# Kernel tuning notes

Hardware: AMD Instinct MI355X
Metric: run time of the kernel (lower is better)

## Reference

```python
import jax, jax.numpy as jnp
import numpy as np
import math

B, N, DIM = 4, 4096, 1024
HEADS, DHEAD, NRF = 16, 64, 64
STAB = 1e-6  # numerical_stabilizer


def setup_inputs() -> dict:
    key = jax.random.key(0)
    k1, k2, k3, k4 = jax.random.split(key, 4)
    x = jax.random.normal(k1, (B, N, DIM), dtype=jnp.float32)
    W_qkv = jax.random.normal(k2, (DIM, 3 * HEADS * DHEAD), dtype=jnp.float32) * (1.0 / math.sqrt(DIM))
    RF = jax.random.normal(k3, (HEADS, DHEAD, NRF), dtype=jnp.float32) / math.sqrt(NRF)
    W_out = jax.random.normal(k4, (HEADS * DHEAD, DIM), dtype=jnp.float32) * (1.0 / math.sqrt(HEADS * DHEAD))
    b_out = jnp.zeros((DIM,), dtype=jnp.float32)
    return {"x": x, "W_qkv": W_qkv, "RF": RF, "W_out": W_out, "b_out": b_out}


def _phi(t, RF):
    # kernel transformation: project onto random features, then ReLU (default kernel)
    return jax.nn.relu(jnp.einsum('bhnd,hdr->bhnr', t, RF))


def reference(x, W_qkv, RF, W_out, b_out):
    b, n, _ = x.shape
    qkv = x @ W_qkv                                  # [b, n, 3*h*d]
    q, k, v = jnp.split(qkv, 3, axis=-1)
    def to_heads(t):
        return t.reshape(b, n, HEADS, DHEAD).transpose(0, 2, 1, 3)  # [b,h,n,d]
    q, k, v = to_heads(q), to_heads(k), to_heads(v)

    phi_q = _phi(q, RF)                              # [b,h,n,r]
    phi_k = _phi(k, RF)                              # [b,h,n,r]

    # linear-complexity FAVOR+ attention
    kv = jnp.einsum('bhnr,bhnd->bhrd', phi_k, v)     # [b,h,r,d]
    out = jnp.einsum('bhnr,bhrd->bhnd', phi_q, kv)   # [b,h,n,d]
    # normalizer: einsum('bhnr,bhmr->bhn') == phi_q @ sum_m(phi_k)
    k_sum = phi_k.sum(axis=2)                        # [b,h,r]
    normalizer = jnp.einsum('bhnr,bhr->bhn', phi_q, k_sum)[..., None] + STAB
    out = out / normalizer

    out = out.transpose(0, 2, 1, 3).reshape(b, n, HEADS * DHEAD)
    out = out @ W_out + b_out
    return out
```

## Files before the change

### kernel.cpp

```cpp
#include <hip/hip_runtime.h>


typedef __attribute__((ext_vector_type(8))) short s8v;
typedef __attribute__((ext_vector_type(4))) short s4v;
typedef __attribute__((ext_vector_type(4))) float f4v;
typedef __attribute__((ext_vector_type(4))) int   i4v;

#define MFMA16(a, b, c) __builtin_amdgcn_mfma_f32_16x16x32_bf16((a), (b), (c), 0, 0, 0)

__device__ __forceinline__ unsigned short f2bf(float f) {
  unsigned int u = __builtin_bit_cast(unsigned int, f);
  unsigned int r = (u + 0x7FFFu + ((u >> 16) & 1u)) >> 16;
  return (unsigned short)r;
}

__device__ __forceinline__ int swz(int p) {
  return p ^ (((p >> 7) & 7) << 4);
}

__device__ __forceinline__ void gl_lds16(const void* g, void* l) {
  __builtin_amdgcn_global_load_lds(
      (const __attribute__((address_space(1))) void*)g,
      (__attribute__((address_space(3))) void*)l, 16, 0, 0);
}

__global__ __launch_bounds__(256) void cvt_bf16(const float* __restrict__ in,
                                                unsigned short* __restrict__ out,
                                                int n4) {
  int i = blockIdx.x * 256 + threadIdx.x;
  if (i >= n4) return;
  f4v v = ((const f4v*)in)[i];
  s4v o;
#pragma unroll
  for (int j = 0; j < 4; ++j) o[j] = (short)f2bf(v[j]);
  ((s4v*)out)[i] = o;
}

__global__ __launch_bounds__(256) void transpose_cvt(const float* __restrict__ in,
                                                     unsigned short* __restrict__ out,
                                                     int R, int C) {
  __shared__ float tile[32][33];
  const int tx = threadIdx.x, ty = threadIdx.y;
  const int z = blockIdx.z;
  const float* inz = in + (size_t)z * R * C;
  unsigned short* outz = out + (size_t)z * R * C;
  const int c0 = blockIdx.x * 32, r0 = blockIdx.y * 32;
#pragma unroll
  for (int j = 0; j < 4; ++j)
    tile[ty + j * 8][tx] = inz[(size_t)(r0 + ty + j * 8) * C + c0 + tx];
  __syncthreads();
#pragma unroll
  for (int j = 0; j < 4; ++j)
    outz[(size_t)(c0 + ty + j * 8) * R + r0 + tx] = f2bf(tile[tx][ty + j * 8]);
}

template <int MODE>
__global__ __launch_bounds__(512, 2) void gemm256(const unsigned short* __restrict__ A,
                                                  const unsigned short* __restrict__ Bt,
                                                  void* __restrict__ Cout,
                                                  const float* __restrict__ bias,
                                                  int Nn, int K, int NTN, int CPX) {
  __shared__ __align__(128) unsigned short smem[65536];
  const int t = threadIdx.x, w = t >> 6, lane = t & 63;
  const int wm = w >> 2, wn = w & 3;
  const int fr = lane & 15, c16 = (lane >> 4) * 16;
  const int nkt = K >> 6;

  const int bid = blockIdx.x;
  const int wg = (bid & 7) * CPX + (bid >> 3);
  const int tm = wg / NTN, tn = wg % NTN;

  const unsigned short* gA = A + (size_t)tm * 256 * K;
  const unsigned short* gB = Bt + (size_t)tn * 256 * K;

  const int s0 = swz(t * 16);
  const int s1 = swz(8192 + t * 16);
  const int goff0 = (s0 >> 7) * K + ((s0 & 127) >> 1);
  const int goff1 = ((s1 - 8192) >> 7) * K + ((s1 & 127) >> 1) + 64 * K;
  const int woff = w * 1024;

  auto stage = [&](int H) {
    if (H >= nkt * 4) return;
    const int TH = H >> 2, part = H & 3;
    char* reg = (char*)smem + (((TH & 1) * 4 + part) << 14);
    const unsigned short* gp =
        (part < 2 ? gA : gB) + (size_t)((part & 1) * 128) * K + TH * 64;
    gl_lds16(gp + goff0, reg + woff);
    gl_lds16(gp + goff1, reg + 8192 + woff);
  };

  f4v acc[8][4] = {};

#pragma unroll
  for (int H = 0; H < 5; ++H) stage(H);
  if (nkt > 1) { asm volatile("s_waitcnt vmcnt(2)" ::: "memory"); }
  else         { asm volatile("s_waitcnt vmcnt(0)" ::: "memory"); }
  __builtin_amdgcn_s_barrier();
  __builtin_amdgcn_sched_barrier(0);

  auto rdA = [&](int mh, s8v (&a)[4][2], const char* Ar) {
#pragma unroll
    for (int i = 0; i < 4; ++i)
#pragma unroll
      for (int ks = 0; ks < 2; ++ks) {
        int p = swz((mh * 64 + i * 16 + fr) * 128 + ks * 64 + c16);
        a[i][ks] = *(const s8v*)(Ar + p);
      }
  };
  auto rdB = [&](int nh, s8v (&b)[2][2], const char* Br, int brow) {
#pragma unroll
    for (int j = 0; j < 2; ++j)
#pragma unroll
      for (int ks = 0; ks < 2; ++ks) {
        int p = swz((brow + nh * 32 + j * 16 + fr) * 128 + ks * 64 + c16);
        b[j][ks] = *(const s8v*)(Br + p);
      }
  };
  auto mmac = [&](int mh, int nh, const s8v (&a)[4][2], const s8v (&b)[2][2]) {
    __builtin_amdgcn_s_setprio(1);
#pragma unroll
    for (int i = 0; i < 4; ++i)
#pragma unroll
      for (int j = 0; j < 2; ++j) {
        acc[mh * 4 + i][nh * 2 + j] = MFMA16(a[i][0], b[j][0], acc[mh * 4 + i][nh * 2 + j]);
        acc[mh * 4 + i][nh * 2 + j] = MFMA16(a[i][1], b[j][1], acc[mh * 4 + i][nh * 2 + j]);
      }
    __builtin_amdgcn_s_setprio(0);
  };

  const int brow = (wn & 1) * 64;
  for (int T = 0; T < nkt; ++T) {
    const int d = T & 1;
    const char* Ar = (const char*)smem + ((d * 4 + wm) << 14);
    const char* Br = (const char*)smem + ((d * 4 + 2 + (wn >> 1)) << 14);
    s8v a[4][2], b0[2][2], b1[2][2];
    rdA(0, a, Ar); rdB(0, b0, Br, brow); stage(4 * T + 5);
    __builtin_amdgcn_s_barrier();
    mmac(0, 0, a, b0);
    __builtin_amdgcn_s_barrier();
    __builtin_amdgcn_sched_barrier(0);
    rdB(1, b1, Br, brow); stage(4 * T + 6);
    __builtin_amdgcn_s_barrier();
    mmac(0, 1, a, b1);
    __builtin_amdgcn_s_barrier();
    __builtin_amdgcn_sched_barrier(0);
    rdA(1, a, Ar); stage(4 * T + 7);
    __builtin_amdgcn_s_barrier();
    mmac(1, 1, a, b1);
    __builtin_amdgcn_s_barrier();
    __builtin_amdgcn_sched_barrier(0);
    stage(4 * T + 8);
    if (T < nkt - 2)       { asm volatile("s_waitcnt vmcnt(2)" ::: "memory"); }
    else if (T == nkt - 2) { asm volatile("s_waitcnt vmcnt(0)" ::: "memory"); }
    __builtin_amdgcn_s_barrier();
    mmac(1, 0, a, b0);
    __builtin_amdgcn_s_barrier();
    __builtin_amdgcn_sched_barrier(0);
  }

#pragma unroll
  for (int m = 0; m < 8; ++m)
#pragma unroll
    for (int n = 0; n < 4; ++n) {
      const int row = tm * 256 + wm * 128 + m * 16 + (lane >> 4) * 4;
      const int col = tn * 256 + wn * 64 + n * 16 + fr;
      if (MODE == 0) {
        unsigned short* C = (unsigned short*)Cout;
#pragma unroll
        for (int r = 0; r < 4; ++r)
          C[(size_t)(row + r) * Nn + col] = f2bf(acc[m][n][r]);
      } else {
        float* C = (float*)Cout;
        const float bv = bias[col];
#pragma unroll
        for (int r = 0; r < 4; ++r)
          C[(size_t)(row + r) * Nn + col] = acc[m][n][r] + bv;
      }
    }
}

__global__ __launch_bounds__(256) void phik_kv(const unsigned short* __restrict__ qkv,
                                               const unsigned short* __restrict__ RFt,
                                               float* __restrict__ kvpart) {
  __shared__ unsigned short RFl[2 * 64 * 32];
  __shared__ unsigned short Kl[2 * 128 * 32];
  __shared__ unsigned short pht[64 * 136];
  __shared__ unsigned short vt[80 * 136];
  const int t = threadIdx.x, w = t >> 6, lane = t & 63;
  const int och = blockIdx.x, h = blockIdx.y, b = blockIdx.z;
  const int fr = lane & 15, kg = (lane >> 4) * 8;

#pragma unroll
  for (int i = 0; i < 2; ++i) {
    int unit = i * 256 + w * 64 + lane;
    int p = unit >> 8, rem = unit & 255;
    int r = rem >> 2, cg = (rem & 3) * 8;
    gl_lds16(RFt + ((h * 64 + r) * 64 + p * 32 + cg), &RFl[(i * 256 + w * 64) * 8]);
  }
  for (int i = t; i < 136; i += 256) vt[64 * 136 + i] = 0x3F80;
  for (int i = t; i < 15 * 136; i += 256) vt[65 * 136 + i] = 0;

  f4v kvacc[5] = {};

  for (int c = 0; c < 4; ++c) {
    const int n0c = och * 512 + c * 128;
    const size_t rowbase = (size_t)(b * 4096 + n0c);
#pragma unroll
    for (int i = 0; i < 4; ++i) {
      int unit = i * 256 + w * 64 + lane;
      int p = unit >> 9, rem = unit & 511;
      int n = rem >> 2, cg = (rem & 3) * 8;
      gl_lds16(qkv + (rowbase + n) * 3072 + 1024 + h * 64 + p * 32 + cg,
               &Kl[(i * 256 + w * 64) * 8]);
    }
    i4v vreg[4];
#pragma unroll
    for (int it = 0; it < 4; ++it) {
      int slot = it * 256 + t;
      vreg[it] = *(const i4v*)&qkv[(rowbase + (slot >> 3)) * 3072 + 2048 + h * 64 +
                                   (slot & 7) * 8];
    }
    __syncthreads();
    f4v pacc[2][4] = {};
#pragma unroll
    for (int p = 0; p < 2; ++p) {
      s8v ka[2], rb[4];
#pragma unroll
      for (int m = 0; m < 2; ++m)
        ka[m] = *(const s8v*)&Kl[p * 4096 + (w * 32 + m * 16 + fr) * 32 + kg];
#pragma unroll
      for (int rf = 0; rf < 4; ++rf)
        rb[rf] = *(const s8v*)&RFl[p * 2048 + (rf * 16 + fr) * 32 + kg];
#pragma unroll
      for (int m = 0; m < 2; ++m)
#pragma unroll
        for (int rf = 0; rf < 4; ++rf)
          pacc[m][rf] = MFMA16(ka[m], rb[rf], pacc[m][rf]);
    }
#pragma unroll
    for (int it = 0; it < 4; ++it) {
      int slot = it * 256 + t;
      int vn = slot >> 3, vdh = (slot & 7) * 8;
      const unsigned short* vr = (const unsigned short*)&vreg[it];
#pragma unroll
      for (int j = 0; j < 8; ++j) vt[(vdh + j) * 136 + vn] = vr[j];
    }
#pragma unroll
    for (int m = 0; m < 2; ++m)
#pragma unroll
      for (int rf = 0; rf < 4; ++rf) {
        int r = rf * 16 + fr;
        int nb = w * 32 + m * 16 + (lane >> 4) * 4;
        s4v pk;
#pragma unroll
        for (int g = 0; g < 4; ++g) pk[g] = (short)f2bf(fmaxf(pacc[m][rf][g], 0.0f));
        *(s4v*)&pht[r * 136 + nb] = pk;
      }
    __syncthreads();
#pragma unroll
    for (int kst = 0; kst < 4; ++kst) {
      s8v pb = *(const s8v*)&pht[(w * 16 + fr) * 136 + kst * 32 + kg];
#pragma unroll
      for (int f = 0; f < 5; ++f) {
        s8v va = *(const s8v*)&vt[(f * 16 + fr) * 136 + kst * 32 + kg];
        kvacc[f] = MFMA16(va, pb, kvacc[f]);
      }
    }
  }
  const int bh = b * 16 + h;
  float* outp = kvpart + ((size_t)bh * 8 + och) * (80 * 64);
#pragma unroll
  for (int f = 0; f < 5; ++f) {
    int row = f * 16 + (lane >> 4) * 4;
    int col = w * 16 + fr;
#pragma unroll
    for (int g = 0; g < 4; ++g) outp[(row + g) * 64 + col] = kvacc[f][g];
  }
}

__global__ __launch_bounds__(256) void kv_reduce(const float* __restrict__ kvpart,
                                                 unsigned short* __restrict__ kvt) {
  const int bh = blockIdx.x, t = threadIdx.x;
  for (int i = t; i < 80 * 64; i += 256) {
    float s = 0.f;
#pragma unroll
    for (int c = 0; c < 8; ++c) s += kvpart[((size_t)bh * 8 + c) * 5120 + i];
    kvt[(size_t)bh * 5120 + i] = f2bf(s);
  }
}

__global__ __launch_bounds__(256) void phiq_out(const unsigned short* __restrict__ qkv,
                                                const unsigned short* __restrict__ RFt,
                                                const unsigned short* __restrict__ kvt,
                                                unsigned short* __restrict__ attno) {
  __shared__ unsigned short RFl[2 * 64 * 32];
  __shared__ unsigned short Ql[2 * 128 * 32];
  __shared__ unsigned short phl[128 * 72];
  __shared__ unsigned short kvl[80 * 72];
  const int t = threadIdx.x, w = t >> 6, lane = t & 63;
  const int ch = blockIdx.x, h = blockIdx.y, b = blockIdx.z;
  const int fr = lane & 15, kg = (lane >> 4) * 8;
  const int bh = b * 16 + h;
  const size_t rowbase = (size_t)(b * 4096 + ch * 128);

#pragma unroll
  for (int i = 0; i < 2; ++i) {
    int unit = i * 256 + w * 64 + lane;
    int p = unit >> 8, rem = unit & 255;
    int r = rem >> 2, cg = (rem & 3) * 8;
    gl_lds16(RFt + ((h * 64 + r) * 64 + p * 32 + cg), &RFl[(i * 256 + w * 64) * 8]);
  }
#pragma unroll
  for (int i = 0; i < 4; ++i) {
    int unit = i * 256 + w * 64 + lane;
    int p = unit >> 9, rem = unit & 511;
    int n = rem >> 2, cg = (rem & 3) * 8;
    gl_lds16(qkv + (rowbase + n) * 3072 + h * 64 + p * 32 + cg,
             &Ql[(i * 256 + w * 64) * 8]);
  }
  for (int i = t; i < 640; i += 256) {
    int row = i >> 3, cg = (i & 7) * 8;
    *(i4v*)&kvl[row * 72 + cg] = *(const i4v*)&kvt[(size_t)bh * 5120 + row * 64 + cg];
  }
  __syncthreads();
  f4v pacc[2][4] = {};
#pragma unroll
  for (int p = 0; p < 2; ++p) {
    s8v qa[2], rb[4];
#pragma unroll
    for (int m = 0; m < 2; ++m)
      qa[m] = *(const s8v*)&Ql[p * 4096 + (w * 32 + m * 16 + fr) * 32 + kg];
#pragma unroll
    for (int rf = 0; rf < 4; ++rf)
      rb[rf] = *(const s8v*)&RFl[p * 2048 + (rf * 16 + fr) * 32 + kg];
#pragma unroll
    for (int m = 0; m < 2; ++m)
#pragma unroll
      for (int rf = 0; rf < 4; ++rf)
        pacc[m][rf] = MFMA16(qa[m], rb[rf], pacc[m][rf]);
  }
#pragma unroll
  for (int m = 0; m < 2; ++m)
#pragma unroll
    for (int rf = 0; rf < 4; ++rf) {
      int r = rf * 16 + fr;
      int nb = w * 32 + m * 16 + (lane >> 4) * 4;
#pragma unroll
      for (int g = 0; g < 4; ++g)
        phl[(nb + g) * 72 + r] = f2bf(fmaxf(pacc[m][rf][g], 0.0f));
    }
  __syncthreads();
  f4v acc[2][5] = {};
#pragma unroll
  for (int kst = 0; kst < 2; ++kst) {
    s8v pa[2], kb[5];
#pragma unroll
    for (int m = 0; m < 2; ++m)
      pa[m] = *(const s8v*)&phl[(w * 32 + m * 16 + fr) * 72 + kst * 32 + kg];
#pragma unroll
    for (int f = 0; f < 5; ++f)
      kb[f] = *(const s8v*)&kvl[(f * 16 + fr) * 72 + kst * 32 + kg];
#pragma unroll
    for (int m = 0; m < 2; ++m)
#pragma unroll
      for (int f = 0; f < 5; ++f) acc[m][f] = MFMA16(pa[m], kb[f], acc[m][f]);
  }
#pragma unroll
  for (int m = 0; m < 2; ++m)
#pragma unroll
    for (int g = 0; g < 4; ++g) {
      float nrm = __shfl(acc[m][4][g], lane & 48) + 1e-6f;
      int n = w * 32 + m * 16 + (lane >> 4) * 4 + g;
      size_t orow = rowbase + n;
#pragma unroll
      for (int f = 0; f < 4; ++f)
        attno[orow * 1024 + h * 64 + f * 16 + fr] = f2bf(acc[m][f][g] / nrm);
    }
}

extern "C" void kernel_launch(void* const* d_in, const int* in_sizes, int n_in,
                              void* d_out, int out_size, void* d_ws, size_t ws_size,
                              hipStream_t stream) {
  const float* x = (const float*)d_in[0];
  const float* W_qkv = (const float*)d_in[1];
  const float* RF = (const float*)d_in[2];
  const float* W_out = (const float*)d_in[3];
  const float* b_out = (const float*)d_in[4];
  float* out = (float*)d_out;

  char* ws = (char*)d_ws;
  size_t off = 0;
  auto alloc = [&](size_t bytes) -> void* {
    void* p = ws + off;
    off += (bytes + 255) & ~(size_t)255;
    return p;
  };
  unsigned short* xb = (unsigned short*)alloc(16384ull * 1024 * 2);
  unsigned short* wqkvt = (unsigned short*)alloc(3072ull * 1024 * 2);
  unsigned short* woutt = (unsigned short*)alloc(1024ull * 1024 * 2);
  unsigned short* rft = (unsigned short*)alloc(16ull * 64 * 64 * 2);
  unsigned short* qkv = (unsigned short*)alloc(16384ull * 3072 * 2);
  float* kvpart = (float*)alloc(64ull * 8 * 80 * 64 * 4);
  unsigned short* kvt = (unsigned short*)alloc(64ull * 80 * 64 * 2);
  unsigned short* attno = (unsigned short*)alloc(16384ull * 1024 * 2);

  cvt_bf16<<<16384, 256, 0, stream>>>(x, xb, 4194304);
  transpose_cvt<<<dim3(96, 32, 1), dim3(32, 8), 0, stream>>>(W_qkv, wqkvt, 1024, 3072);
  transpose_cvt<<<dim3(32, 32, 1), dim3(32, 8), 0, stream>>>(W_out, woutt, 1024, 1024);
  transpose_cvt<<<dim3(2, 2, 16), dim3(32, 8), 0, stream>>>(RF, rft, 64, 64);

  gemm256<0><<<768, 512, 0, stream>>>(xb, wqkvt, qkv, nullptr, 3072, 1024, 12, 96);
  phik_kv<<<dim3(8, 16, 4), 256, 0, stream>>>(qkv, rft, kvpart);
  kv_reduce<<<64, 256, 0, stream>>>(kvpart, kvt);
  phiq_out<<<dim3(32, 16, 4), 256, 0, stream>>>(qkv, rft, kvt, attno);
  gemm256<1><<<256, 512, 0, stream>>>(attno, woutt, out, b_out, 1024, 1024, 4, 32);
}
```

Baseline: 229.1 us.

## Prefetch B tiles two steps ahead and vectorize GEMM epilogue stores

The GEMM prefetch schedule changes so the B-operand halves of the next-next k-tile are issued one step earlier, with the vmcnt waits raised from 2 to 4 to match the deeper pipeline. The MFMA operands are swapped so each lane holds four consecutive columns of a row, which lets the epilogue write 4 bf16 or 4 fp32 values per store instead of scalar strided stores. This is meant to hide more global-load latency and cut store instruction count and uncoalesced writes, at the cost of more loads in flight.

```diff
diff --git a/kernel.cpp b/kernel.cpp
--- a/kernel.cpp
+++ b/kernel.cpp
@@ -79,21 +79,20 @@
   const int goff1 = ((s1 - 8192) >> 7) * K + ((s1 & 127) >> 1) + 64 * K;
   const int woff = w * 1024;
 
-  auto stage = [&](int H) {
-    if (H >= nkt * 4) return;
-    const int TH = H >> 2, part = H & 3;
-    char* reg = (char*)smem + (((TH & 1) * 4 + part) << 14);
+  auto stage = [&](int T2, int part) {
+    if (T2 >= nkt) return;
+    char* reg = (char*)smem + (((T2 & 1) * 4 + part) << 14);
     const unsigned short* gp =
-        (part < 2 ? gA : gB) + (size_t)((part & 1) * 128) * K + TH * 64;
+        (part < 2 ? gA : gB) + (size_t)((part & 1) * 128) * K + T2 * 64;
     gl_lds16(gp + goff0, reg + woff);
     gl_lds16(gp + goff1, reg + 8192 + woff);
   };
 
   f4v acc[8][4] = {};
 
-#pragma unroll
-  for (int H = 0; H < 5; ++H) stage(H);
-  if (nkt > 1) { asm volatile("s_waitcnt vmcnt(2)" ::: "memory"); }
+  stage(0, 0); stage(0, 1); stage(0, 2); stage(0, 3);
+  stage(1, 2); stage(1, 3);
+  if (nkt > 1) { asm volatile("s_waitcnt vmcnt(4)" ::: "memory"); }
   else         { asm volatile("s_waitcnt vmcnt(0)" ::: "memory"); }
   __builtin_amdgcn_s_barrier();
   __builtin_amdgcn_sched_barrier(0);
@@ -122,8 +121,8 @@
     for (int i = 0; i < 4; ++i)
 #pragma unroll
       for (int j = 0; j < 2; ++j) {
-        acc[mh * 4 + i][nh * 2 + j] = MFMA16(a[i][0], b[j][0], acc[mh * 4 + i][nh * 2 + j]);
-        acc[mh * 4 + i][nh * 2 + j] = MFMA16(a[i][1], b[j][1], acc[mh * 4 + i][nh * 2 + j]);
+        acc[mh * 4 + i][nh * 2 + j] = MFMA16(b[j][0], a[i][0], acc[mh * 4 + i][nh * 2 + j]);
+        acc[mh * 4 + i][nh * 2 + j] = MFMA16(b[j][1], a[i][1], acc[mh * 4 + i][nh * 2 + j]);
       }
     __builtin_amdgcn_s_setprio(0);
   };
@@ -134,23 +133,23 @@
     const char* Ar = (const char*)smem + ((d * 4 + wm) << 14);
     const char* Br = (const char*)smem + ((d * 4 + 2 + (wn >> 1)) << 14);
     s8v a[4][2], b0[2][2], b1[2][2];
-    rdA(0, a, Ar); rdB(0, b0, Br, brow); stage(4 * T + 5);
+    rdA(0, a, Ar); rdB(0, b0, Br, brow); stage(T + 1, 0);
     __builtin_amdgcn_s_barrier();
     mmac(0, 0, a, b0);
     __builtin_amdgcn_s_barrier();
     __builtin_amdgcn_sched_barrier(0);
-    rdB(1, b1, Br, brow); stage(4 * T + 6);
+    rdB(1, b1, Br, brow); stage(T + 1, 1);
     __builtin_amdgcn_s_barrier();
     mmac(0, 1, a, b1);
     __builtin_amdgcn_s_barrier();
     __builtin_amdgcn_sched_barrier(0);
-    rdA(1, a, Ar); stage(4 * T + 7);
+    rdA(1, a, Ar); stage(T + 2, 2);
     __builtin_amdgcn_s_barrier();
     mmac(1, 1, a, b1);
     __builtin_amdgcn_s_barrier();
     __builtin_amdgcn_sched_barrier(0);
-    stage(4 * T + 8);
-    if (T < nkt - 2)       { asm volatile("s_waitcnt vmcnt(2)" ::: "memory"); }
+    stage(T + 2, 3);
+    if (T < nkt - 2)       { asm volatile("s_waitcnt vmcnt(4)" ::: "memory"); }
     else if (T == nkt - 2) { asm volatile("s_waitcnt vmcnt(0)" ::: "memory"); }
     __builtin_amdgcn_s_barrier();
     mmac(1, 0, a, b0);
@@ -162,19 +161,19 @@
   for (int m = 0; m < 8; ++m)
 #pragma unroll
     for (int n = 0; n < 4; ++n) {
-      const int row = tm * 256 + wm * 128 + m * 16 + (lane >> 4) * 4;
-      const int col = tn * 256 + wn * 64 + n * 16 + fr;
+      const int row = tm * 256 + wm * 128 + m * 16 + fr;
+      const int col = tn * 256 + wn * 64 + n * 16 + (lane >> 4) * 4;
       if (MODE == 0) {
         unsigned short* C = (unsigned short*)Cout;
-#pragma unroll
-        for (int r = 0; r < 4; ++r)
-          C[(size_t)(row + r) * Nn + col] = f2bf(acc[m][n][r]);
+        s4v o;
+#pragma unroll
+        for (int g = 0; g < 4; ++g) o[g] = (short)f2bf(acc[m][n][g]);
+        *(s4v*)&C[(size_t)row * Nn + col] = o;
       } else {
         float* C = (float*)Cout;
-        const float bv = bias[col];
-#pragma unroll
-        for (int r = 0; r < 4; ++r)
-          C[(size_t)(row + r) * Nn + col] = acc[m][n][r] + bv;
+        const f4v bv = *(const f4v*)&bias[col];
+        f4v o = acc[m][n] + bv;
+        *(f4v*)&C[(size_t)row * Nn + col] = o;
       }
     }
 }
```

Measured after the change: 242.4 us. 5.8% more time.
